# Optimization experiments

Hardware: AMD Instinct MI355X
Metric: run time of the kernel (lower is better)

## Reference

```python
import jax, jax.numpy as jnp
import numpy as np

RATIO = 0.25
RS = (0.2, 0.4)       # ball-query radii per scale
NS = (32, 64)         # max neighbors per scale
NEG = -1e30


def setup_inputs() -> dict:
    key = jax.random.key(0)
    ks = jax.random.split(key, 10)
    B, P, C = 4, 8192, 64
    pos = jax.random.uniform(ks[0], (B, P, 3), dtype=jnp.float32)
    x = jax.random.normal(ks[1], (B, P, C), dtype=jnp.float32)

    def lin(k, i, o):
        return jax.random.normal(k, (i, o), dtype=jnp.float32) / np.float32(np.sqrt(i))

    return {
        "x": x, "pos": pos,
        "w1_0": lin(ks[2], C + 3, 64),  "b1_0": jnp.zeros((64,), jnp.float32),
        "w1_1": lin(ks[3], 64, 128),    "b1_1": jnp.zeros((128,), jnp.float32),
        "w2_0": lin(ks[4], C + 3, 128), "b2_0": jnp.zeros((128,), jnp.float32),
        "w2_1": lin(ks[5], 128, 256),   "b2_1": jnp.zeros((256,), jnp.float32),
    }


def fps(pos_b, m):
    """Farthest point sampling on one cloud [P,3] -> [m] int32 indices (start at 0)."""
    P = pos_b.shape[0]

    def step(carry, _):
        mind, last = carry
        d = jnp.sum((pos_b - pos_b[last]) ** 2, axis=-1)   # [P]
        mind = jnp.minimum(mind, d)
        nxt = jnp.argmax(mind).astype(jnp.int32)
        return (mind, nxt), last

    init = (jnp.full((P,), 1e30, pos_b.dtype), jnp.array(0, jnp.int32))
    _, idx = jax.lax.scan(step, init, None, length=m)
    return idx


def reference(x, pos, w1_0, b1_0, w1_1, b1_1, w2_0, b2_0, w2_1, b2_1):
    B, P, C = x.shape
    M = int(P * RATIO)
    idx = jax.vmap(lambda p: fps(p, M))(pos)                       # [B, M]
    pos_s = jnp.take_along_axis(pos, idx[..., None], axis=1)       # [B, M, 3]

    # pairwise squared distances centroid -> all points, per batch   [B, M, P]
    d2 = jnp.sum((pos_s[:, :, None, :] - pos[:, None, :, :]) ** 2, axis=-1)

    gather = jax.vmap(lambda a, i: a[i])  # ([P,*],[M,K]) -> [M,K,*]
    branches = [((w1_0, w1_1), (b1_0, b1_1)), ((w2_0, w2_1), (b2_0, b2_1))]
    outs = []
    for (r, K, (ws, bs)) in zip(RS, NS, branches):
        negd, nidx = jax.lax.top_k(-d2, K)         # K nearest; [B, M, K]
        mask = (-negd) <= r * r                    # within ball  [B, M, K]
        xj = gather(x, nidx)                       # [B, M, K, C]
        pj = gather(pos, nidx)                     # [B, M, K, 3]
        h = jnp.concatenate([xj, pj - pos_s[:, :, None, :]], axis=-1)
        for W, b in zip(ws, bs):
            h = jax.nn.relu(h @ W + b)
        h = jnp.where(mask[..., None], h, NEG)
        outs.append(jnp.max(h, axis=2))            # max aggregation over neighbors
    out = jnp.concatenate(outs, axis=-1)           # [B, M, 384]
    return out, pos_s
```

## Files before the change

kernel.cpp:

```cpp
#include <hip/hip_runtime.h>
#include <stdint.h>

#define BATCH 4
#define NPTS  8192
#define CFEAT 64
#define MCENT 2048
#define NCENT (BATCH * MCENT)
#define KMAX  64
#define NEGV  -1e30f
#define KNN_CAP 320
#define PROG_STRIDE 32

__device__ __forceinline__ float dist2(float ax, float ay, float az,
                                       float bx, float by, float bz) {
    float dx = __fsub_rn(ax, bx);
    float dy = __fsub_rn(ay, by);
    float dz = __fsub_rn(az, bz);
    return __fadd_rn(__fadd_rn(__fmul_rn(dx, dx), __fmul_rn(dy, dy)),
                     __fmul_rn(dz, dz));
}

template <int CTRL>
__device__ __forceinline__ int dppi(int v) {
    return __builtin_amdgcn_update_dpp(v, v, CTRL, 0xF, 0xF, false);
}

#define KSTEP(k, C_) { int klo_ = dppi<C_>((int)(unsigned int)(k));           \
                       int khi_ = dppi<C_>((int)(unsigned int)((k) >> 32));   \
                       unsigned long long ok_ =                               \
                           ((unsigned long long)(unsigned int)khi_ << 32) |   \
                           (unsigned int)klo_;                                \
                       (k) = ok_ > (k) ? ok_ : (k); }

struct FpsLds {
    float2 sxy[NPTS];
    float  sz[NPTS];
    int    s_win[MCENT];
    unsigned long long skey[2][4];
};
struct KnnLds {
    float4 p3[KMAX];
    float  H[KMAX * 128];
    unsigned long long cand[KNN_CAP];
    float  pm2[4][256];
    float  pm[256];
    int    hist[64];
    int    nbr[KMAX];
    float  nd2s[KMAX];
    float  ctr[4];
    int    B64, total, cnt2, cntk;
};
union MegaLds { FpsLds f; KnnLds k; };

template <int K, int C1, int C2, int OUTOFF>
__device__ __forceinline__ void mlp_phase(
        KnnLds& L, const float* __restrict__ x,
        const float* __restrict__ W1, const float* __restrict__ B1,
        const float* __restrict__ W2, const float* __restrict__ B2,
        float* __restrict__ out, float r2, int c, int b, int t) {
    constexpr int HK  = K / 8;
    constexpr int NJ1 = C1 / 32;
    {
        const int hw = t >> 5;
        const int sl = t & 31;
        const int k0 = hw * HK;
        const int j0 = sl * NJ1;

        int xo[HK];
#pragma unroll
        for (int kk = 0; kk < HK; ++kk)
            xo[kk] = (b * NPTS + L.nbr[k0 + kk]) * CFEAT;

        float acc[HK][NJ1];
#pragma unroll
        for (int kk = 0; kk < HK; ++kk)
#pragma unroll
            for (int j = 0; j < NJ1; ++j) acc[kk][j] = B1[j0 + j];

#pragma unroll 4
        for (int q = 0; q < 16; ++q) {
            float wr[4][NJ1];
#pragma unroll
            for (int r = 0; r < 4; ++r)
#pragma unroll
                for (int j = 0; j < NJ1; ++j)
                    wr[r][j] = W1[(4 * q + r) * C1 + j0 + j];
#pragma unroll
            for (int kk = 0; kk < HK; ++kk) {
                float4 h = *(const float4*)(x + xo[kk] + 4 * q);
#pragma unroll
                for (int j = 0; j < NJ1; ++j) {
                    float a = acc[kk][j];
                    a = fmaf(h.x, wr[0][j], a);
                    a = fmaf(h.y, wr[1][j], a);
                    a = fmaf(h.z, wr[2][j], a);
                    a = fmaf(h.w, wr[3][j], a);
                    acc[kk][j] = a;
                }
            }
        }
        {
            float wr[4][NJ1];
#pragma unroll
            for (int r = 0; r < 3; ++r)
#pragma unroll
                for (int j = 0; j < NJ1; ++j)
                    wr[r][j] = W1[(64 + r) * C1 + j0 + j];
#pragma unroll
            for (int j = 0; j < NJ1; ++j) wr[3][j] = 0.f;
#pragma unroll
            for (int kk = 0; kk < HK; ++kk) {
                float4 h = L.p3[k0 + kk];
#pragma unroll
                for (int j = 0; j < NJ1; ++j) {
                    float a = acc[kk][j];
                    a = fmaf(h.x, wr[0][j], a);
                    a = fmaf(h.y, wr[1][j], a);
                    a = fmaf(h.z, wr[2][j], a);
                    a = fmaf(h.w, wr[3][j], a);
                    acc[kk][j] = a;
                }
            }
        }
#pragma unroll
        for (int kk = 0; kk < HK; ++kk) {
            if constexpr (NJ1 == 4) {
                float4 o;
                o.x = fmaxf(acc[kk][0], 0.f); o.y = fmaxf(acc[kk][1], 0.f);
                o.z = fmaxf(acc[kk][2], 0.f); o.w = fmaxf(acc[kk][3], 0.f);
                *(float4*)&L.H[(k0 + kk) * C1 + j0] = o;
            } else {
                float2 o;
                o.x = fmaxf(acc[kk][0], 0.f); o.y = fmaxf(acc[kk][1], 0.f);
                *(float2*)&L.H[(k0 + kk) * C1 + j0] = o;
            }
        }
    }
    __syncthreads();

    const int cntk = L.cntk;
    const int cntp = cntk < K ? cntk : K;

    if constexpr (C2 == 256) {
        const int lane_ = t & 63;
        const int wv_   = t >> 6;
        const int j0    = lane_ * 4;
        const int k0    = wv_ * (K / 4);
        float4 bjv = *(const float4*)&B2[j0];
        float acc[K / 4][4];
#pragma unroll
        for (int kk = 0; kk < K / 4; ++kk) {
            acc[kk][0] = bjv.x; acc[kk][1] = bjv.y;
            acc[kk][2] = bjv.z; acc[kk][3] = bjv.w;
        }
        for (int i = 0; i < C1; i += 4) {
            float4 w0 = *(const float4*)&W2[(i + 0) * C2 + j0];
            float4 w1 = *(const float4*)&W2[(i + 1) * C2 + j0];
            float4 w2 = *(const float4*)&W2[(i + 2) * C2 + j0];
            float4 w3 = *(const float4*)&W2[(i + 3) * C2 + j0];
#pragma unroll
            for (int kk = 0; kk < K / 4; ++kk) {
                float4 h = *(const float4*)&L.H[(k0 + kk) * C1 + i];
                acc[kk][0] = fmaf(h.x, w0.x, acc[kk][0]);
                acc[kk][0] = fmaf(h.y, w1.x, acc[kk][0]);
                acc[kk][0] = fmaf(h.z, w2.x, acc[kk][0]);
                acc[kk][0] = fmaf(h.w, w3.x, acc[kk][0]);
                acc[kk][1] = fmaf(h.x, w0.y, acc[kk][1]);
                acc[kk][1] = fmaf(h.y, w1.y, acc[kk][1]);
                acc[kk][1] = fmaf(h.z, w2.y, acc[kk][1]);
                acc[kk][1] = fmaf(h.w, w3.y, acc[kk][1]);
                acc[kk][2] = fmaf(h.x, w0.z, acc[kk][2]);
                acc[kk][2] = fmaf(h.y, w1.z, acc[kk][2]);
                acc[kk][2] = fmaf(h.z, w2.z, acc[kk][2]);
                acc[kk][2] = fmaf(h.w, w3.z, acc[kk][2]);
                acc[kk][3] = fmaf(h.x, w0.w, acc[kk][3]);
                acc[kk][3] = fmaf(h.y, w1.w, acc[kk][3]);
                acc[kk][3] = fmaf(h.z, w2.w, acc[kk][3]);
                acc[kk][3] = fmaf(h.w, w3.w, acc[kk][3]);
            }
        }
        float m0 = NEGV, m1 = NEGV, m2 = NEGV, m3 = NEGV;
#pragma unroll
        for (int kk = 0; kk < K / 4; ++kk) {
            bool v = (k0 + kk < cntp) && (L.nd2s[k0 + kk] <= r2);
            if (v) {
                m0 = fmaxf(m0, fmaxf(acc[kk][0], 0.f));
                m1 = fmaxf(m1, fmaxf(acc[kk][1], 0.f));
                m2 = fmaxf(m2, fmaxf(acc[kk][2], 0.f));
                m3 = fmaxf(m3, fmaxf(acc[kk][3], 0.f));
            }
        }
        float4 mv; mv.x = m0; mv.y = m1; mv.z = m2; mv.w = m3;
        *(float4*)&L.pm2[wv_][j0] = mv;
        __syncthreads();
        float r = fmaxf(fmaxf(L.pm2[0][t], L.pm2[1][t]),
                        fmaxf(L.pm2[2][t], L.pm2[3][t]));
        out[c * 384 + OUTOFF + t] = r;
    } else {
        const int j2 = t % C2;
        const int g  = t / C2;
        float w2c[C1];
#pragma unroll
        for (int i = 0; i < C1; ++i) w2c[i] = W2[i * C2 + j2];
        const float bj = B2[j2];
        float omax = NEGV;
        for (int k = g; k < K; k += 2) {
            bool v = (k < cntp) && (L.nd2s[k] <= r2);
            if (!v) continue;
            float acc = bj;
            const float4* hr = (const float4*)&L.H[k * C1];
#pragma unroll
            for (int q = 0; q < C1 / 4; ++q) {
                float4 h = hr[q];
                acc = fmaf(h.x, w2c[4 * q + 0], acc);
                acc = fmaf(h.y, w2c[4 * q + 1], acc);
                acc = fmaf(h.z, w2c[4 * q + 2], acc);
                acc = fmaf(h.w, w2c[4 * q + 3], acc);
            }
            omax = fmaxf(omax, fmaxf(acc, 0.f));
        }
        L.pm[t] = omax;
        __syncthreads();
        if (t < C2) out[c * 384 + OUTOFF + t] = fmaxf(L.pm[t], L.pm[t + C2]);
    }
}

#define FPS_T   256
#define FPS_W   (FPS_T / 64)

#define REP32(X) X(0) X(1) X(2) X(3) X(4) X(5) X(6) X(7) \
                 X(8) X(9) X(10) X(11) X(12) X(13) X(14) X(15) \
                 X(16) X(17) X(18) X(19) X(20) X(21) X(22) X(23) \
                 X(24) X(25) X(26) X(27) X(28) X(29) X(30) X(31)

__global__ __launch_bounds__(256, 1) void mega_kernel(
        const float* __restrict__ x, const float* __restrict__ pos,
        const float* __restrict__ w1_0, const float* __restrict__ b1_0,
        const float* __restrict__ w1_1, const float* __restrict__ b1_1,
        const float* __restrict__ w2_0, const float* __restrict__ b2_0,
        const float* __restrict__ w2_1, const float* __restrict__ b2_1,
        float* __restrict__ out, float* pos_s, int* prog) {
    const int t = threadIdx.x;
    __shared__ MegaLds U;

    if (blockIdx.x < BATCH) {
        const int b = blockIdx.x;
        const float* pb = pos + b * NPTS * 3;
        const int w = t >> 6;
        const int lane = t & 63;

#define FPS_DECL(i) float px##i, py##i, pz##i, mind##i;
        REP32(FPS_DECL)
#undef FPS_DECL

#define FPS_LOAD(i) { int p = (i << 8) + t;                                   \
                      px##i = pb[3 * p + 0];                                  \
                      py##i = pb[3 * p + 1];                                  \
                      pz##i = pb[3 * p + 2];                                  \
                      float2 xy_; xy_.x = px##i; xy_.y = py##i;               \
                      U.f.sxy[p] = xy_;  U.f.sz[p] = pz##i;                   \
                      mind##i = 1e30f;                                        \
                      asm volatile("" : "+v"(px##i), "+v"(py##i), "+v"(pz##i)); }
        REP32(FPS_LOAD)
#undef FPS_LOAD
        if (t == 0) U.f.s_win[0] = 0;
        __syncthreads();

        float lx = U.f.sxy[0].x, ly = U.f.sxy[0].y, lz = U.f.sz[0];

        for (int m = 0; m < MCENT - 1; ++m) {
#define FPS_UPD(i) { float d = dist2(px##i, py##i, pz##i, lx, ly, lz);        \
                     mind##i = fminf(mind##i, d); }
            REP32(FPS_UPD)
#undef FPS_UPD

#define CMB(vo, io, va, ia, vb, ib)                                           \
            float vo; int io; { bool tk_ = (vb) > (va);                       \
                                vo = tk_ ? (vb) : (va);                       \
                                io = tk_ ? (ib) : (ia); }
            CMB(A0v,A0i,  mind0,0,   mind1,1)   CMB(A1v,A1i,  mind2,2,   mind3,3)
            CMB(A2v,A2i,  mind4,4,   mind5,5)   CMB(A3v,A3i,  mind6,6,   mind7,7)
            CMB(A4v,A4i,  mind8,8,   mind9,9)   CMB(A5v,A5i,  mind10,10, mind11,11)
            CMB(A6v,A6i,  mind12,12, mind13,13) CMB(A7v,A7i,  mind14,14, mind15,15)
            CMB(A8v,A8i,  mind16,16, mind17,17) CMB(A9v,A9i,  mind18,18, mind19,19)
            CMB(A10v,A10i,mind20,20, mind21,21) CMB(A11v,A11i,mind22,22, mind23,23)
            CMB(A12v,A12i,mind24,24, mind25,25) CMB(A13v,A13i,mind26,26, mind27,27)
            CMB(A14v,A14i,mind28,28, mind29,29) CMB(A15v,A15i,mind30,30, mind31,31)
            CMB(B0v,B0i, A0v,A0i,  A1v,A1i)   CMB(B1v,B1i, A2v,A2i,  A3v,A3i)
            CMB(B2v,B2i, A4v,A4i,  A5v,A5i)   CMB(B3v,B3i, A6v,A6i,  A7v,A7i)
            CMB(B4v,B4i, A8v,A8i,  A9v,A9i)   CMB(B5v,B5i, A10v,A10i,A11v,A11i)
            CMB(B6v,B6i, A12v,A12i,A13v,A13i) CMB(B7v,B7i, A14v,A14i,A15v,A15i)
            CMB(C0v,C0i, B0v,B0i, B1v,B1i)    CMB(C1v,C1i, B2v,B2i, B3v,B3i)
            CMB(C2v,C2i, B4v,B4i, B5v,B5i)    CMB(C3v,C3i, B6v,B6i, B7v,B7i)
            CMB(D0v,D0i, C0v,C0i, C1v,C1i)    CMB(D1v,D1i, C2v,C2i, C3v,C3i)
            CMB(E0v,E0i, D0v,D0i, D1v,D1i)
#undef CMB
            const float bv = E0v;
            const int   bp = (E0i << 8) + t;

            unsigned long long key =
                ((unsigned long long)__float_as_uint(bv) << 13) |
                (unsigned int)(8191 - bp);
            KSTEP(key, 0xB1)
            KSTEP(key, 0x4E)
            KSTEP(key, 0x141)
            KSTEP(key, 0x140)
            KSTEP(key, 0x142)
            KSTEP(key, 0x143)

            const int par = m & 1;
            if (lane == 63) U.f.skey[par][w] = key;
            __syncthreads();

            unsigned long long k = U.f.skey[par][t & 3];
            KSTEP(k, 0xB1)
            KSTEP(k, 0x4E)

            int gp = 8191 - (int)(k & 0x1FFFULL);
            if (t == 0) {
                U.f.s_win[m + 1] = gp;
                if ((m & 63) == 63) {
                    float* o = pos_s + (b * MCENT + (m - 63)) * 3;
                    for (int q = 0; q < 64; ++q) {
                        int gq = U.f.s_win[m - 63 + q];
                        float2 xy = U.f.sxy[gq];
                        float  z  = U.f.sz[gq];
                        o[3 * q + 0] = xy.x;
                        o[3 * q + 1] = xy.y;
                        o[3 * q + 2] = z;
                    }
                    __hip_atomic_store(&prog[b * PROG_STRIDE], m + 1,
                                       __ATOMIC_RELEASE,
                                       __HIP_MEMORY_SCOPE_AGENT);
                }
            }
            float2 cxy = U.f.sxy[gp];
            lx = cxy.x; ly = cxy.y; lz = U.f.sz[gp];
        }

        if (t == 0) {
            float* o = pos_s + (b * MCENT + (MCENT - 64)) * 3;
            for (int q = 0; q < 64; ++q) {
                int gq = U.f.s_win[MCENT - 64 + q];
                float2 xy = U.f.sxy[gq];
                float  z  = U.f.sz[gq];
                o[3 * q + 0] = xy.x;
                o[3 * q + 1] = xy.y;
                o[3 * q + 2] = z;
            }
            __hip_atomic_store(&prog[b * PROG_STRIDE], MCENT,
                               __ATOMIC_RELEASE, __HIP_MEMORY_SCOPE_AGENT);
        }
        return;
    }

    const int idx = blockIdx.x - BATCH;
    const int b   = idx & 3;
    const int m   = idx >> 2;
    const int c   = b * MCENT + m;
    KnnLds& L = U.k;
    const float* pb = pos + b * NPTS * 3;

    if (t < KMAX) { L.nbr[t] = 0; L.nd2s[t] = 1e30f; L.hist[t] = 0; }
    if (t == 0) L.cnt2 = 0;

    if (t == 0) {
        int tries = 0;
        while (__hip_atomic_load(&prog[b * PROG_STRIDE], __ATOMIC_RELAXED,
                                 __HIP_MEMORY_SCOPE_AGENT) < m + 1) {
            __builtin_amdgcn_s_sleep(32);
            if (++tries >= (1 << 18)) break;
        }
        asm volatile("" ::: "memory");
        L.ctr[0] = __hip_atomic_load(&pos_s[c * 3 + 0], __ATOMIC_RELAXED,
                                     __HIP_MEMORY_SCOPE_AGENT);
        L.ctr[1] = __hip_atomic_load(&pos_s[c * 3 + 1], __ATOMIC_RELAXED,
                                     __HIP_MEMORY_SCOPE_AGENT);
        L.ctr[2] = __hip_atomic_load(&pos_s[c * 3 + 2], __ATOMIC_RELAXED,
                                     __HIP_MEMORY_SCOPE_AGENT);
    }
    __syncthreads();
    const float cx = L.ctr[0], cy = L.ctr[1], cz = L.ctr[2];

    float d2r[32];
#pragma unroll
    for (int i = 0; i < 32; ++i) {
        int p = (i << 8) + t;
        float d2 = dist2(cx, cy, cz, pb[3 * p + 0], pb[3 * p + 1], pb[3 * p + 2]);
        d2r[i] = d2;
        if (d2 <= 0.16f) {
            int bkt = (int)(d2 * 400.0f);
            bkt = bkt > 63 ? 63 : bkt;
            atomicAdd(&L.hist[bkt], 1);
        }
    }
    __syncthreads();
    if (t == 0) {
        int cum = 0, B = -1;
#pragma unroll
        for (int j = 0; j < 64; ++j) {
            cum += L.hist[j];
            if (B < 0 && cum >= 64) B = j;
        }
        L.B64 = (B < 0) ? 63 : B;
        L.total = cum;
    }
    __syncthreads();
    const int B64 = L.B64;
#pragma unroll
    for (int i = 0; i < 32; ++i) {
        float d2 = d2r[i];
        if (d2 <= 0.16f) {
            int bkt = (int)(d2 * 400.0f);
            bkt = bkt > 63 ? 63 : bkt;
            if (bkt <= B64) {
                int slot = atomicAdd(&L.cnt2, 1);
                if (slot < KNN_CAP) {
                    int p = (i << 8) + t;
                    L.cand[slot] =
                        ((unsigned long long)__float_as_uint(d2) << 32) |
                        (unsigned int)p;
                }
            }
        }
    }
    __syncthreads();
    const int C = L.cnt2 < KNN_CAP ? L.cnt2 : KNN_CAP;
    for (int tc = t; tc < C; tc += 256) {
        unsigned long long my = L.cand[tc];
        int rank = 0;
        for (int j = 0; j < C; ++j) rank += (L.cand[j] < my) ? 1 : 0;
        if (rank < KMAX) {
            L.nbr[rank]  = (int)(my & 0xffffffffULL);
            L.nd2s[rank] = __uint_as_float((unsigned int)(my >> 32));
        }
    }
    if (t == 0) L.cntk = L.total < KMAX ? L.total : KMAX;
    __syncthreads();
    if (t < KMAX) {
        const float* pp = pos + (b * NPTS + L.nbr[t]) * 3;
        float4 p;
        p.x = pp[0] - cx; p.y = pp[1] - cy; p.z = pp[2] - cz; p.w = 0.f;
        L.p3[t] = p;
    }
    __syncthreads();

    mlp_phase<32, 64, 128, 0>(L, x, w1_0, b1_0, w1_1, b1_1, out, 0.04f, c, b, t);
    __syncthreads();
    mlp_phase<64, 128, 256, 128>(L, x, w2_0, b2_0, w2_1, b2_1, out, 0.16f, c, b, t);
}
#undef KSTEP

extern "C" void kernel_launch(void* const* d_in, const int* in_sizes, int n_in,
                              void* d_out, int out_size, void* d_ws, size_t ws_size,
                              hipStream_t stream) {
    const float* x    = (const float*)d_in[0];
    const float* pos  = (const float*)d_in[1];
    const float* w1_0 = (const float*)d_in[2];
    const float* b1_0 = (const float*)d_in[3];
    const float* w1_1 = (const float*)d_in[4];
    const float* b1_1 = (const float*)d_in[5];
    const float* w2_0 = (const float*)d_in[6];
    const float* b2_0 = (const float*)d_in[7];
    const float* w2_1 = (const float*)d_in[8];
    const float* b2_1 = (const float*)d_in[9];

    float* out   = (float*)d_out;
    float* pos_s = out + NCENT * 384;

    int* prog = (int*)d_ws;

    hipMemsetAsync(prog, 0, BATCH * PROG_STRIDE * sizeof(int), stream);
    mega_kernel<<<BATCH + NCENT, 256, 0, stream>>>(
        x, pos, w1_0, b1_0, w1_1, b1_1, w2_0, b2_0, w2_1, b2_1,
        out, pos_s, prog);
}
```

Before: 2.166 ms.

## Widen mega kernel blocks to 512 threads and streamline FPS argmax

Raises the block size from 256 to 512 threads, so each FPS thread holds 16 points instead of 32. The per-thread argmax is folded into the distance update loop as a running compare instead of a separate tree reduction, and the cross-wave reduction gains one more DPP step to cover 8 waves. The KNN and MLP phases are adapted: the MLP runs only on the first 256 threads, and the 256-wide layer is split into two chunks of 8 neighbours to cut register pressure for launch_bounds(512,2). The aim is a shorter serial FPS critical path and more occupancy, at the cost of idle threads in the MLP and an extra barrier-wide reduction step.

New measurement: 2.065 ms. 4.7% less time.

```diff
diff --git a/kernel.cpp b/kernel.cpp
--- a/kernel.cpp
+++ b/kernel.cpp
@@ -36,7 +36,7 @@
     float2 sxy[NPTS];
     float  sz[NPTS];
     int    s_win[MCENT];
-    unsigned long long skey[2][4];
+    unsigned long long skey[2][8];
 };
 struct KnnLds {
     float4 p3[KMAX];
@@ -60,7 +60,8 @@
         float* __restrict__ out, float r2, int c, int b, int t) {
     constexpr int HK  = K / 8;
     constexpr int NJ1 = C1 / 32;
-    {
+    const bool act = t < 256;
+    if (act) {
         const int hw = t >> 5;
         const int sl = t & 31;
         const int k0 = hw * HK;
@@ -142,98 +143,105 @@
     const int cntp = cntk < K ? cntk : K;
 
     if constexpr (C2 == 256) {
-        const int lane_ = t & 63;
-        const int wv_   = t >> 6;
-        const int j0    = lane_ * 4;
-        const int k0    = wv_ * (K / 4);
-        float4 bjv = *(const float4*)&B2[j0];
-        float acc[K / 4][4];
-#pragma unroll
-        for (int kk = 0; kk < K / 4; ++kk) {
-            acc[kk][0] = bjv.x; acc[kk][1] = bjv.y;
-            acc[kk][2] = bjv.z; acc[kk][3] = bjv.w;
-        }
-        for (int i = 0; i < C1; i += 4) {
-            float4 w0 = *(const float4*)&W2[(i + 0) * C2 + j0];
-            float4 w1 = *(const float4*)&W2[(i + 1) * C2 + j0];
-            float4 w2 = *(const float4*)&W2[(i + 2) * C2 + j0];
-            float4 w3 = *(const float4*)&W2[(i + 3) * C2 + j0];
-#pragma unroll
-            for (int kk = 0; kk < K / 4; ++kk) {
-                float4 h = *(const float4*)&L.H[(k0 + kk) * C1 + i];
-                acc[kk][0] = fmaf(h.x, w0.x, acc[kk][0]);
-                acc[kk][0] = fmaf(h.y, w1.x, acc[kk][0]);
-                acc[kk][0] = fmaf(h.z, w2.x, acc[kk][0]);
-                acc[kk][0] = fmaf(h.w, w3.x, acc[kk][0]);
-                acc[kk][1] = fmaf(h.x, w0.y, acc[kk][1]);
-                acc[kk][1] = fmaf(h.y, w1.y, acc[kk][1]);
-                acc[kk][1] = fmaf(h.z, w2.y, acc[kk][1]);
-                acc[kk][1] = fmaf(h.w, w3.y, acc[kk][1]);
-                acc[kk][2] = fmaf(h.x, w0.z, acc[kk][2]);
-                acc[kk][2] = fmaf(h.y, w1.z, acc[kk][2]);
-                acc[kk][2] = fmaf(h.z, w2.z, acc[kk][2]);
-                acc[kk][2] = fmaf(h.w, w3.z, acc[kk][2]);
-                acc[kk][3] = fmaf(h.x, w0.w, acc[kk][3]);
-                acc[kk][3] = fmaf(h.y, w1.w, acc[kk][3]);
-                acc[kk][3] = fmaf(h.z, w2.w, acc[kk][3]);
-                acc[kk][3] = fmaf(h.w, w3.w, acc[kk][3]);
-            }
-        }
-        float m0 = NEGV, m1 = NEGV, m2 = NEGV, m3 = NEGV;
-#pragma unroll
-        for (int kk = 0; kk < K / 4; ++kk) {
-            bool v = (k0 + kk < cntp) && (L.nd2s[k0 + kk] <= r2);
-            if (v) {
-                m0 = fmaxf(m0, fmaxf(acc[kk][0], 0.f));
-                m1 = fmaxf(m1, fmaxf(acc[kk][1], 0.f));
-                m2 = fmaxf(m2, fmaxf(acc[kk][2], 0.f));
-                m3 = fmaxf(m3, fmaxf(acc[kk][3], 0.f));
-            }
-        }
-        float4 mv; mv.x = m0; mv.y = m1; mv.z = m2; mv.w = m3;
-        *(float4*)&L.pm2[wv_][j0] = mv;
+        if (act) {
+            const int lane_ = t & 63;
+            const int wv_   = t >> 6;
+            const int j0    = lane_ * 4;
+            float4 bjv = *(const float4*)&B2[j0];
+            float mx0 = NEGV, mx1 = NEGV, mx2 = NEGV, mx3 = NEGV;
+#pragma unroll
+            for (int ch = 0; ch < 2; ++ch) {
+                const int k0 = wv_ * (K / 4) + ch * 8;
+                float acc[8][4];
+#pragma unroll
+                for (int kk = 0; kk < 8; ++kk) {
+                    acc[kk][0] = bjv.x; acc[kk][1] = bjv.y;
+                    acc[kk][2] = bjv.z; acc[kk][3] = bjv.w;
+                }
+                for (int i = 0; i < C1; i += 4) {
+                    float4 w0 = *(const float4*)&W2[(i + 0) * C2 + j0];
+                    float4 w1 = *(const float4*)&W2[(i + 1) * C2 + j0];
+                    float4 w2 = *(const float4*)&W2[(i + 2) * C2 + j0];
+                    float4 w3 = *(const float4*)&W2[(i + 3) * C2 + j0];
+#pragma unroll
+                    for (int kk = 0; kk < 8; ++kk) {
+                        float4 h = *(const float4*)&L.H[(k0 + kk) * C1 + i];
+                        acc[kk][0] = fmaf(h.x, w0.x, acc[kk][0]);
+                        acc[kk][0] = fmaf(h.y, w1.x, acc[kk][0]);
+                        acc[kk][0] = fmaf(h.z, w2.x, acc[kk][0]);
+                        acc[kk][0] = fmaf(h.w, w3.x, acc[kk][0]);
+                        acc[kk][1] = fmaf(h.x, w0.y, acc[kk][1]);
+                        acc[kk][1] = fmaf(h.y, w1.y, acc[kk][1]);
+                        acc[kk][1] = fmaf(h.z, w2.y, acc[kk][1]);
+                        acc[kk][1] = fmaf(h.w, w3.y, acc[kk][1]);
+                        acc[kk][2] = fmaf(h.x, w0.z, acc[kk][2]);
+                        acc[kk][2] = fmaf(h.y, w1.z, acc[kk][2]);
+                        acc[kk][2] = fmaf(h.z, w2.z, acc[kk][2]);
+                        acc[kk][2] = fmaf(h.w, w3.z, acc[kk][2]);
+                        acc[kk][3] = fmaf(h.x, w0.w, acc[kk][3]);
+                        acc[kk][3] = fmaf(h.y, w1.w, acc[kk][3]);
+                        acc[kk][3] = fmaf(h.z, w2.w, acc[kk][3]);
+                        acc[kk][3] = fmaf(h.w, w3.w, acc[kk][3]);
+                    }
+                }
+#pragma unroll
+                for (int kk = 0; kk < 8; ++kk) {
+                    bool v = (k0 + kk < cntp) && (L.nd2s[k0 + kk] <= r2);
+                    if (v) {
+                        mx0 = fmaxf(mx0, fmaxf(acc[kk][0], 0.f));
+                        mx1 = fmaxf(mx1, fmaxf(acc[kk][1], 0.f));
+                        mx2 = fmaxf(mx2, fmaxf(acc[kk][2], 0.f));
+                        mx3 = fmaxf(mx3, fmaxf(acc[kk][3], 0.f));
+                    }
+                }
+            }
+            float4 mv; mv.x = mx0; mv.y = mx1; mv.z = mx2; mv.w = mx3;
+            *(float4*)&L.pm2[wv_][j0] = mv;
+        }
         __syncthreads();
-        float r = fmaxf(fmaxf(L.pm2[0][t], L.pm2[1][t]),
-                        fmaxf(L.pm2[2][t], L.pm2[3][t]));
-        out[c * 384 + OUTOFF + t] = r;
+        if (t < C2) {
+            float r = fmaxf(fmaxf(L.pm2[0][t], L.pm2[1][t]),
+                            fmaxf(L.pm2[2][t], L.pm2[3][t]));
+            out[c * 384 + OUTOFF + t] = r;
+        }
     } else {
-        const int j2 = t % C2;
-        const int g  = t / C2;
-        float w2c[C1];
-#pragma unroll
-        for (int i = 0; i < C1; ++i) w2c[i] = W2[i * C2 + j2];
-        const float bj = B2[j2];
-        float omax = NEGV;
-        for (int k = g; k < K; k += 2) {
-            bool v = (k < cntp) && (L.nd2s[k] <= r2);
-            if (!v) continue;
-            float acc = bj;
-            const float4* hr = (const float4*)&L.H[k * C1];
-#pragma unroll
-            for (int q = 0; q < C1 / 4; ++q) {
-                float4 h = hr[q];
-                acc = fmaf(h.x, w2c[4 * q + 0], acc);
-                acc = fmaf(h.y, w2c[4 * q + 1], acc);
-                acc = fmaf(h.z, w2c[4 * q + 2], acc);
-                acc = fmaf(h.w, w2c[4 * q + 3], acc);
-            }
-            omax = fmaxf(omax, fmaxf(acc, 0.f));
-        }
-        L.pm[t] = omax;
+        if (act) {
+            const int j2 = t % C2;
+            const int g  = t / C2;
+            float w2c[C1];
+#pragma unroll
+            for (int i = 0; i < C1; ++i) w2c[i] = W2[i * C2 + j2];
+            const float bj = B2[j2];
+            float omax = NEGV;
+            for (int k = g; k < K; k += 2) {
+                bool v = (k < cntp) && (L.nd2s[k] <= r2);
+                if (!v) continue;
+                float acc = bj;
+                const float4* hr = (const float4*)&L.H[k * C1];
+#pragma unroll
+                for (int q = 0; q < C1 / 4; ++q) {
+                    float4 h = hr[q];
+                    acc = fmaf(h.x, w2c[4 * q + 0], acc);
+                    acc = fmaf(h.y, w2c[4 * q + 1], acc);
+                    acc = fmaf(h.z, w2c[4 * q + 2], acc);
+                    acc = fmaf(h.w, w2c[4 * q + 3], acc);
+                }
+                omax = fmaxf(omax, fmaxf(acc, 0.f));
+            }
+            L.pm[t] = omax;
+        }
         __syncthreads();
         if (t < C2) out[c * 384 + OUTOFF + t] = fmaxf(L.pm[t], L.pm[t + C2]);
     }
 }
 
-#define FPS_T   256
+#define FPS_T   512
 #define FPS_W   (FPS_T / 64)
 
-#define REP32(X) X(0) X(1) X(2) X(3) X(4) X(5) X(6) X(7) \
-                 X(8) X(9) X(10) X(11) X(12) X(13) X(14) X(15) \
-                 X(16) X(17) X(18) X(19) X(20) X(21) X(22) X(23) \
-                 X(24) X(25) X(26) X(27) X(28) X(29) X(30) X(31)
-
-__global__ __launch_bounds__(256, 1) void mega_kernel(
+#define REP16(X) X(0) X(1) X(2) X(3) X(4) X(5) X(6) X(7) \
+                 X(8) X(9) X(10) X(11) X(12) X(13) X(14) X(15)
+
+__global__ __launch_bounds__(FPS_T, 2) void mega_kernel(
         const float* __restrict__ x, const float* __restrict__ pos,
         const float* __restrict__ w1_0, const float* __restrict__ b1_0,
         const float* __restrict__ w1_1, const float* __restrict__ b1_1,
@@ -250,10 +258,10 @@
         const int lane = t & 63;
 
 #define FPS_DECL(i) float px##i, py##i, pz##i, mind##i;
-        REP32(FPS_DECL)
+        REP16(FPS_DECL)
 #undef FPS_DECL
 
-#define FPS_LOAD(i) { int p = (i << 8) + t;                                   \
+#define FPS_LOAD(i) { int p = (i << 9) + t;                                   \
                       px##i = pb[3 * p + 0];                                  \
                       py##i = pb[3 * p + 1];                                  \
                       pz##i = pb[3 * p + 2];                                  \
@@ -261,7 +269,7 @@
                       U.f.sxy[p] = xy_;  U.f.sz[p] = pz##i;                   \
                       mind##i = 1e30f;                                        \
                       asm volatile("" : "+v"(px##i), "+v"(py##i), "+v"(pz##i)); }
-        REP32(FPS_LOAD)
+        REP16(FPS_LOAD)
 #undef FPS_LOAD
         if (t == 0) U.f.s_win[0] = 0;
         __syncthreads();
@@ -269,34 +277,16 @@
         float lx = U.f.sxy[0].x, ly = U.f.sxy[0].y, lz = U.f.sz[0];
 
         for (int m = 0; m < MCENT - 1; ++m) {
+            float bv = -1.0f; int bi = 0;
 #define FPS_UPD(i) { float d = dist2(px##i, py##i, pz##i, lx, ly, lz);        \
-                     mind##i = fminf(mind##i, d); }
-            REP32(FPS_UPD)
+                     float mn = fminf(mind##i, d);                            \
+                     mind##i = mn;                                            \
+                     bool tk = mn > bv;                                       \
+                     bv = tk ? mn : bv;                                       \
+                     bi = tk ? i : bi; }
+            REP16(FPS_UPD)
 #undef FPS_UPD
-
-#define CMB(vo, io, va, ia, vb, ib)                                           \
-            float vo; int io; { bool tk_ = (vb) > (va);                       \
-                                vo = tk_ ? (vb) : (va);                       \
-                                io = tk_ ? (ib) : (ia); }
-            CMB(A0v,A0i,  mind0,0,   mind1,1)   CMB(A1v,A1i,  mind2,2,   mind3,3)
-            CMB(A2v,A2i,  mind4,4,   mind5,5)   CMB(A3v,A3i,  mind6,6,   mind7,7)
-            CMB(A4v,A4i,  mind8,8,   mind9,9)   CMB(A5v,A5i,  mind10,10, mind11,11)
-            CMB(A6v,A6i,  mind12,12, mind13,13) CMB(A7v,A7i,  mind14,14, mind15,15)
-            CMB(A8v,A8i,  mind16,16, mind17,17) CMB(A9v,A9i,  mind18,18, mind19,19)
-            CMB(A10v,A10i,mind20,20, mind21,21) CMB(A11v,A11i,mind22,22, mind23,23)
-            CMB(A12v,A12i,mind24,24, mind25,25) CMB(A13v,A13i,mind26,26, mind27,27)
-            CMB(A14v,A14i,mind28,28, mind29,29) CMB(A15v,A15i,mind30,30, mind31,31)
-            CMB(B0v,B0i, A0v,A0i,  A1v,A1i)   CMB(B1v,B1i, A2v,A2i,  A3v,A3i)
-            CMB(B2v,B2i, A4v,A4i,  A5v,A5i)   CMB(B3v,B3i, A6v,A6i,  A7v,A7i)
-            CMB(B4v,B4i, A8v,A8i,  A9v,A9i)   CMB(B5v,B5i, A10v,A10i,A11v,A11i)
-            CMB(B6v,B6i, A12v,A12i,A13v,A13i) CMB(B7v,B7i, A14v,A14i,A15v,A15i)
-            CMB(C0v,C0i, B0v,B0i, B1v,B1i)    CMB(C1v,C1i, B2v,B2i, B3v,B3i)
-            CMB(C2v,C2i, B4v,B4i, B5v,B5i)    CMB(C3v,C3i, B6v,B6i, B7v,B7i)
-            CMB(D0v,D0i, C0v,C0i, C1v,C1i)    CMB(D1v,D1i, C2v,C2i, C3v,C3i)
-            CMB(E0v,E0i, D0v,D0i, D1v,D1i)
-#undef CMB
-            const float bv = E0v;
-            const int   bp = (E0i << 8) + t;
+            int bp = (bi << 9) + t;
 
             unsigned long long key =
                 ((unsigned long long)__float_as_uint(bv) << 13) |
@@ -312,9 +302,10 @@
             if (lane == 63) U.f.skey[par][w] = key;
             __syncthreads();
 
-            unsigned long long k = U.f.skey[par][t & 3];
+            unsigned long long k = U.f.skey[par][t & 7];
             KSTEP(k, 0xB1)
             KSTEP(k, 0x4E)
+            KSTEP(k, 0x141)
 
             int gp = 8191 - (int)(k & 0x1FFFULL);
             if (t == 0) {
@@ -382,10 +373,10 @@
     __syncthreads();
     const float cx = L.ctr[0], cy = L.ctr[1], cz = L.ctr[2];
 
-    float d2r[32];
-#pragma unroll
-    for (int i = 0; i < 32; ++i) {
-        int p = (i << 8) + t;
+    float d2r[16];
+#pragma unroll
+    for (int i = 0; i < 16; ++i) {
+        int p = (i << 9) + t;
         float d2 = dist2(cx, cy, cz, pb[3 * p + 0], pb[3 * p + 1], pb[3 * p + 2]);
         d2r[i] = d2;
         if (d2 <= 0.16f) {
@@ -408,7 +399,7 @@
     __syncthreads();
     const int B64 = L.B64;
 #pragma unroll
-    for (int i = 0; i < 32; ++i) {
+    for (int i = 0; i < 16; ++i) {
         float d2 = d2r[i];
         if (d2 <= 0.16f) {
             int bkt = (int)(d2 * 400.0f);
@@ -416,7 +407,7 @@
             if (bkt <= B64) {
                 int slot = atomicAdd(&L.cnt2, 1);
                 if (slot < KNN_CAP) {
-                    int p = (i << 8) + t;
+                    int p = (i << 9) + t;
                     L.cand[slot] =
                         ((unsigned long long)__float_as_uint(d2) << 32) |
                         (unsigned int)p;
@@ -426,7 +417,7 @@
     }
     __syncthreads();
     const int C = L.cnt2 < KNN_CAP ? L.cnt2 : KNN_CAP;
-    for (int tc = t; tc < C; tc += 256) {
+    for (int tc = t; tc < C; tc += 512) {
         unsigned long long my = L.cand[tc];
         int rank = 0;
         for (int j = 0; j < C; ++j) rank += (L.cand[j] < my) ? 1 : 0;
@@ -471,7 +462,7 @@
     int* prog = (int*)d_ws;
 
     hipMemsetAsync(prog, 0, BATCH * PROG_STRIDE * sizeof(int), stream);
-    mega_kernel<<<BATCH + NCENT, 256, 0, stream>>>(
+    mega_kernel<<<BATCH + NCENT, FPS_T, 0, stream>>>(
         x, pos, w1_0, b1_0, w1_1, b1_1, w2_0, b2_0, w2_1, b2_1,
         out, pos_s, prog);
 }
```
